# Kernel optimization log

Hardware: AMD Instinct MI355X
Metric: run time of the kernel (lower is better)

The kernel has to match this reference:

```python
import jax, jax.numpy as jnp
import numpy as np

CODEBOOK_DIM = 64
CODEBOOK_SLOTS = 512
TEMPERATURE = 0.5
BS, H, W = 16, 64, 64
EPS_G = 1e-10  # gumbel numerical floor
EPS_P = 1e-9   # matches probs.add(1e-09) in torch code


def setup_inputs() -> dict:
    key = jax.random.key(0)
    k1, k2, k3 = jax.random.split(key, 3)
    ze = jax.random.normal(k1, (BS, CODEBOOK_DIM, H, W), dtype=jnp.float32)
    codebook = jax.random.normal(k2, (CODEBOOK_SLOTS, CODEBOOK_DIM), dtype=jnp.float32)
    # uniform noise for Gumbel reparameterization of RelaxedOneHotCategorical.rsample
    u = jax.random.uniform(k3, (BS * H * W, CODEBOOK_SLOTS), dtype=jnp.float32)
    return {"ze": ze, "codebook": codebook, "u": u}


def reference(ze, codebook, u):
    bs, d, h, w = ze.shape
    K = codebook.shape[0]
    log_K = jnp.log(jnp.float32(K))
    # [bs, d, h, w] -> [N, d]
    ze_flat = jnp.transpose(ze, (0, 2, 3, 1)).reshape(-1, d)
    # squared euclidean distances via addmm: ||c||^2 + ||z||^2 - 2 z c^T  -> [N, K]
    distances = (
        jnp.sum(codebook * codebook, axis=1)[None, :]
        + jnp.sum(ze_flat * ze_flat, axis=1, keepdims=True)
        - 2.0 * (ze_flat @ codebook.T)
    )
    logits = -distances
    # Gumbel-softmax (relaxed one-hot categorical rsample)
    gumbel = -jnp.log(-jnp.log(u + EPS_G) + EPS_G)
    soft_onehot = jax.nn.softmax((logits + gumbel) / TEMPERATURE, axis=1)
    hard_indices = jnp.argmax(soft_onehot, axis=1).reshape(bs, h, w)
    # weighted codebook lookup: [N, K] @ [K, d] -> [bs, h, w, d] -> [bs, d, h, w]
    z_q = jnp.transpose((soft_onehot @ codebook).reshape(bs, h, w, d), (0, 3, 1, 2))
    probs = jax.nn.softmax(logits, axis=1)
    KL = jnp.mean(jnp.sum((probs * (jnp.log(probs + EPS_P) + log_K)).reshape(bs, -1), axis=1))
    commit_loss = jnp.mean(jnp.sum((probs * distances).reshape(bs, -1), axis=1))
    return (z_q, hard_indices, KL, commit_loss)
```

## Files before the change

### kernel.cpp

```cpp
#include <hip/hip_runtime.h>
#include <math.h>
#include <stdint.h>

#define IDX_OFF 4194304
#define KL_OFF  4259840
#define CM_OFF  4259841
#define LOG_K   6.238324625039508f
#define THR     2.0f

typedef _Float16 half8 __attribute__((ext_vector_type(8)));
typedef _Float16 half4 __attribute__((ext_vector_type(4)));
typedef float    f32x4 __attribute__((ext_vector_type(4)));

__global__ __launch_bounds__(64) void vq_pack(const float* __restrict__ cbk, void* __restrict__ ws){
  _Float16* LAh = (_Float16*)ws;
  _Float16* LAl = LAh + 32768;
  _Float16* QAh = LAl + 32768;
  float*    CCw = (float*)(QAh + 32768);
  const int slot = blockIdx.x, c = threadIdx.x;
  const float x = cbk[(slot << 6) + c];
  const _Float16 h = (_Float16)x;
  const _Float16 l = (_Float16)(x - (float)h);
  const int g = slot >> 4;
  {
    const int kc = c >> 5, quad = (c >> 3) & 3, j = c & 7;
    const int lane = (quad << 4) | (slot & 15);
    const int idx = ((((g << 1) | kc) << 6) | lane) * 8 + j;
    LAh[idx] = h; LAl[idx] = l;
  }
  {
    const int quad2 = (slot >> 2) & 3, j2 = slot & 3;
    const int cg = c >> 4;
    const int lane = (quad2 << 4) | (c & 15);
    QAh[(((g << 6) | lane) << 4) | (cg << 2) | j2] = h;
  }
  float s = x * x;
#pragma unroll
  for (int m = 1; m < 64; m <<= 1) s += __shfl_xor(s, m, 64);
  if (c == 0) CCw[slot] = s;
}

__global__ __launch_bounds__(512, 3) void vq_main(
    const float* __restrict__ ze, const float* __restrict__ uin,
    const void* __restrict__ ws, float* __restrict__ out)
{
  __shared__ float LX[4*22*64];
  __shared__ float RED[8];
  const _Float16* wsp = (const _Float16*)ws;
  const half8* LAh = (const half8*)wsp;
  const half8* LAl = (const half8*)(wsp + 32768);
  const half8* QA8 = (const half8*)(wsp + 65536);
  const float* CCw = (const float*)(wsp + 98304);

  const int tid  = threadIdx.x;
  const int lane = tid & 63, l15 = lane & 15, quad = lane >> 4;
  const int wv   = tid >> 6, pg = wv & 3, half = wv >> 2;
  const int n    = (blockIdx.x << 6) | (pg << 4) | l15;
  const int bb   = n >> 12, hh = (n >> 6) & 63, w = n & 63;

  const float* zp = ze + ((size_t)bb << 18) + (hh << 6) + w;
  half8 zh[2], zl[2];
  float zz = 0.f;
#pragma unroll
  for (int kc = 0; kc < 2; ++kc)
#pragma unroll
    for (int j = 0; j < 8; ++j){
      const float x = zp[(size_t)((kc << 5) + (quad << 3) + j) << 12];
      zz = fmaf(x, x, zz);
      const _Float16 h = (_Float16)x;
      zh[kc][j] = h;
      zl[kc][j] = (_Float16)(x - (float)h);
    }
  zz += __shfl_xor(zz, 16, 64);
  zz += __shfl_xor(zz, 32, 64);

  float m1 = -3.0e38f, s1 = 0.f, s2s = 0.f, t1s = 0.f, am = -3.0e38f;
  int   ki = 0;
  f32x4 zq0 = {0.f,0.f,0.f,0.f}, zq1 = {0.f,0.f,0.f,0.f};
  f32x4 zq2 = {0.f,0.f,0.f,0.f}, zq3 = {0.f,0.f,0.f,0.f};

  const float* uB = uin + ((size_t)n << 9) + (half << 8) + (quad << 2);
  const int gbase = half << 4;

#pragma unroll 2
  for (int g = 0; g < 16; ++g){
    const int gl = gbase + g;
    const float4 uf = *(const float4*)(uB + (g << 4));
    const float4 c4 = *(const float4*)(CCw + (gl << 4) + (quad << 2));
    const half8 ch0 = LAh[((gl << 1) | 0) * 64 + lane];
    const half8 ch1 = LAh[((gl << 1) | 1) * 64 + lane];
    const half8 cl0 = LAl[((gl << 1) | 0) * 64 + lane];
    const half8 cl1 = LAl[((gl << 1) | 1) * 64 + lane];
    const half8 qa01 = QA8[((gl << 6) | lane) * 2 + 0];
    const half8 qa23 = QA8[((gl << 6) | lane) * 2 + 1];

    f32x4 acc = {0.f,0.f,0.f,0.f};
    acc = __builtin_amdgcn_mfma_f32_16x16x32_f16(ch0, zh[0], acc, 0,0,0);
    acc = __builtin_amdgcn_mfma_f32_16x16x32_f16(cl0, zh[0], acc, 0,0,0);
    acc = __builtin_amdgcn_mfma_f32_16x16x32_f16(ch0, zl[0], acc, 0,0,0);
    acc = __builtin_amdgcn_mfma_f32_16x16x32_f16(ch1, zh[1], acc, 0,0,0);
    acc = __builtin_amdgcn_mfma_f32_16x16x32_f16(cl1, zh[1], acc, 0,0,0);
    acc = __builtin_amdgcn_mfma_f32_16x16x32_f16(ch1, zl[1], acc, 0,0,0);

    const float ua[4] = {uf.x, uf.y, uf.z, uf.w};
    const float ca[4] = {c4.x, c4.y, c4.z, c4.w};
    float lg[4], lu[4], av[4];
#pragma unroll
    for (int r = 0; r < 4; ++r){
      lg[r] = fmaf(2.f, acc[r], -ca[r] - zz);
      lu[r] = 1e-10f - __logf(ua[r] + 1e-10f);
      av[r] = lg[r] - __logf(lu[r]);
    }
    float pm = fmaxf(fmaxf(av[0], av[1]), fmaxf(av[2], av[3]));
    pm = fmaxf(pm, __shfl_xor(pm, 16, 64));
    pm = fmaxf(pm, __shfl_xor(pm, 32, 64));
    if (pm > m1 + THR){
      const float sc = __expf(m1 - pm), sc2 = sc * sc;
      s1 *= sc2; s2s *= sc; t1s *= sc;
      zq0 *= sc2; zq1 *= sc2; zq2 *= sc2; zq3 *= sc2;
      m1 = pm;
    }
    half4 ef;
    const int sb = (gl << 4) | (quad << 2);
#pragma unroll
    for (int r = 0; r < 4; ++r){
      const float t = __expf(av[r] - m1);
      const float e = t * t;
      s1 += e;
      ef[r] = (_Float16)e;
      const float p = t * lu[r];
      s2s += p;
      t1s = fmaf(p, lg[r], t1s);
      if (av[r] > am){ am = av[r]; ki = sb + r; }
    }
    const half4 qa0 = __builtin_shufflevector(qa01, qa01, 0,1,2,3);
    const half4 qa1 = __builtin_shufflevector(qa01, qa01, 4,5,6,7);
    const half4 qa2 = __builtin_shufflevector(qa23, qa23, 0,1,2,3);
    const half4 qa3 = __builtin_shufflevector(qa23, qa23, 4,5,6,7);
    zq0 = __builtin_amdgcn_mfma_f32_16x16x16f16(qa0, ef, zq0, 0,0,0);
    zq1 = __builtin_amdgcn_mfma_f32_16x16x16f16(qa1, ef, zq1, 0,0,0);
    zq2 = __builtin_amdgcn_mfma_f32_16x16x16f16(qa2, ef, zq2, 0,0,0);
    zq3 = __builtin_amdgcn_mfma_f32_16x16x16f16(qa3, ef, zq3, 0,0,0);
  }

#pragma unroll
  for (int m = 16; m < 64; m <<= 1){
    s1  += __shfl_xor(s1,  m, 64);
    s2s += __shfl_xor(s2s, m, 64);
    t1s += __shfl_xor(t1s, m, 64);
    const float vo = __shfl_xor(am, m, 64);
    const int   io = __shfl_xor(ki, m, 64);
    if (vo > am || (vo == am && io < ki)){ am = vo; ki = io; }
  }

  float* X = &LX[(pg * 22) * 64 + lane];
  if (half == 1){
#pragma unroll
    for (int r = 0; r < 4; ++r){
      X[(r     ) << 6] = zq0[r];
      X[(r +  4) << 6] = zq1[r];
      X[(r +  8) << 6] = zq2[r];
      X[(r + 12) << 6] = zq3[r];
    }
    X[16 << 6] = s1;  X[17 << 6] = s2s; X[18 << 6] = t1s;
    X[19 << 6] = m1;  X[20 << 6] = am;  X[21 << 6] = __int_as_float(ki);
  }
  __syncthreads();
  if (half == 0){
    const float m1B = X[19 << 6];
    const float M   = fmaxf(m1, m1B);
    const float sA  = __expf(m1 - M),  sB  = __expf(m1B - M);
    const float sA2 = sA * sA,         sB2 = sB * sB;
    s1  = s1  * sA2 + X[16 << 6] * sB2;
    s2s = s2s * sA  + X[17 << 6] * sB;
    t1s = t1s * sA  + X[18 << 6] * sB;
    const float amB = X[20 << 6];
    const int   kiB = __float_as_int(X[21 << 6]);
    if (amB > am || (amB == am && kiB < ki)){ am = amB; ki = kiB; }
    m1 = M;
#pragma unroll
    for (int r = 0; r < 4; ++r){
      zq0[r] = zq0[r] * sA2 + X[(r     ) << 6] * sB2;
      zq1[r] = zq1[r] * sA2 + X[(r +  4) << 6] * sB2;
      zq2[r] = zq2[r] * sA2 + X[(r +  8) << 6] * sB2;
      zq3[r] = zq3[r] * sA2 + X[(r + 12) << 6] * sB2;
    }

    const float inv = 1.0f / s1;
    const float pl  = t1s / s2s;
    float kl = pl + LOG_K - m1 - __logf(s2s);
    float cm = -pl;
    if (quad == 0) out[IDX_OFF + n] = (float)ki;

    float* ob = out + ((size_t)bb << 18) + (hh << 6) + w;
#pragma unroll
    for (int r = 0; r < 4; ++r){
      const int cb = (quad << 2) + r;
      ob[(size_t)(cb     ) << 12] = zq0[r] * inv;
      ob[(size_t)(cb + 16) << 12] = zq1[r] * inv;
      ob[(size_t)(cb + 32) << 12] = zq2[r] * inv;
      ob[(size_t)(cb + 48) << 12] = zq3[r] * inv;
    }

    if (quad != 0){ kl = 0.f; cm = 0.f; }
#pragma unroll
    for (int m = 1; m < 64; m <<= 1){ kl += __shfl_xor(kl, m, 64); cm += __shfl_xor(cm, m, 64); }
    if (lane == 0){ RED[pg] = kl; RED[pg + 4] = cm; }
  }
  __syncthreads();
  if (tid == 0){
    atomicAdd(out + KL_OFF, (RED[0]+RED[1]+RED[2]+RED[3]) * 0.0625f);
    atomicAdd(out + CM_OFF, (RED[4]+RED[5]+RED[6]+RED[7]) * 0.0625f);
  }
}

extern "C" void kernel_launch(void* const* d_in, const int* in_sizes, int n_in,
                              void* d_out, int out_size, void* d_ws, size_t ws_size,
                              hipStream_t stream){
  const float* ze  = (const float*)d_in[0];
  const float* cbk = (const float*)d_in[1];
  const float* uin = (const float*)d_in[2];
  float* out = (float*)d_out;
  hipMemsetAsync(out + KL_OFF, 0, 2 * sizeof(float), stream);
  vq_pack<<<dim3(512), dim3(64), 0, stream>>>(cbk, d_ws);
  vq_main<<<dim3(1024), dim3(512), 0, stream>>>(ze, uin, d_ws, out);
}
```

Before: 249.0 us.

## Software-pipeline codebook and noise loads and shrink blocks to 256 threads

Adds register double-buffering so each loop iteration already holds its codebook fragments and uniform noise, prefetching the next group's codebook data and the noise two groups ahead. Blocks now cover 32 points with 4 waves instead of 64 points with 8, and the grid doubles with adjusted launch bounds. The aim is to hide global/L2 load latency behind MFMA and transcendental work and to give the scheduler more, smaller blocks. In exchange it raises register pressure, which can cut occupancy, and the last iterations issue wrapped-around loads that are never used.

```diff
diff --git a/kernel.cpp b/kernel.cpp
--- a/kernel.cpp
+++ b/kernel.cpp
@@ -40,12 +40,12 @@
   if (c == 0) CCw[slot] = s;
 }
 
-__global__ __launch_bounds__(512, 3) void vq_main(
+__global__ __launch_bounds__(256, 4) void vq_main(
     const float* __restrict__ ze, const float* __restrict__ uin,
     const void* __restrict__ ws, float* __restrict__ out)
 {
-  __shared__ float LX[4*22*64];
-  __shared__ float RED[8];
+  __shared__ float LX[2*22*64];
+  __shared__ float RED[4];
   const _Float16* wsp = (const _Float16*)ws;
   const half8* LAh = (const half8*)wsp;
   const half8* LAl = (const half8*)(wsp + 32768);
@@ -54,8 +54,8 @@
 
   const int tid  = threadIdx.x;
   const int lane = tid & 63, l15 = lane & 15, quad = lane >> 4;
-  const int wv   = tid >> 6, pg = wv & 3, half = wv >> 2;
-  const int n    = (blockIdx.x << 6) | (pg << 4) | l15;
+  const int wv   = tid >> 6, pg = wv & 1, half = wv >> 1;
+  const int n    = (blockIdx.x << 5) | (pg << 4) | l15;
   const int bb   = n >> 12, hh = (n >> 6) & 63, w = n & 63;
 
   const float* zp = ze + ((size_t)bb << 18) + (hh << 6) + w;
@@ -82,28 +82,40 @@
   const float* uB = uin + ((size_t)n << 9) + (half << 8) + (quad << 2);
   const int gbase = half << 4;
 
-#pragma unroll 2
+  float4 ufc = *(const float4*)(uB);
+  float4 uf1 = *(const float4*)(uB + 16);
+  float4 c4c = *(const float4*)(CCw + (gbase << 4) + (quad << 2));
+  half8 ch0c = LAh[((gbase << 1) | 0) * 64 + lane];
+  half8 ch1c = LAh[((gbase << 1) | 1) * 64 + lane];
+  half8 cl0c = LAl[((gbase << 1) | 0) * 64 + lane];
+  half8 cl1c = LAl[((gbase << 1) | 1) * 64 + lane];
+  half8 qa01c = QA8[((gbase << 6) | lane) * 2 + 0];
+  half8 qa23c = QA8[((gbase << 6) | lane) * 2 + 1];
+
+#pragma unroll 4
   for (int g = 0; g < 16; ++g){
-    const int gl = gbase + g;
-    const float4 uf = *(const float4*)(uB + (g << 4));
-    const float4 c4 = *(const float4*)(CCw + (gl << 4) + (quad << 2));
-    const half8 ch0 = LAh[((gl << 1) | 0) * 64 + lane];
-    const half8 ch1 = LAh[((gl << 1) | 1) * 64 + lane];
-    const half8 cl0 = LAl[((gl << 1) | 0) * 64 + lane];
-    const half8 cl1 = LAl[((gl << 1) | 1) * 64 + lane];
-    const half8 qa01 = QA8[((gl << 6) | lane) * 2 + 0];
-    const half8 qa23 = QA8[((gl << 6) | lane) * 2 + 1];
+    const int g1 = (g + 1) & 15, g2 = (g + 2) & 15;
+    const int gl  = gbase + g;
+    const int gl1 = gbase + g1;
+    const float4 uf2 = *(const float4*)(uB + (g2 << 4));
+    const float4 c4n = *(const float4*)(CCw + (gl1 << 4) + (quad << 2));
+    const half8 ch0n = LAh[((gl1 << 1) | 0) * 64 + lane];
+    const half8 ch1n = LAh[((gl1 << 1) | 1) * 64 + lane];
+    const half8 cl0n = LAl[((gl1 << 1) | 0) * 64 + lane];
+    const half8 cl1n = LAl[((gl1 << 1) | 1) * 64 + lane];
+    const half8 qa01n = QA8[((gl1 << 6) | lane) * 2 + 0];
+    const half8 qa23n = QA8[((gl1 << 6) | lane) * 2 + 1];
 
     f32x4 acc = {0.f,0.f,0.f,0.f};
-    acc = __builtin_amdgcn_mfma_f32_16x16x32_f16(ch0, zh[0], acc, 0,0,0);
-    acc = __builtin_amdgcn_mfma_f32_16x16x32_f16(cl0, zh[0], acc, 0,0,0);
-    acc = __builtin_amdgcn_mfma_f32_16x16x32_f16(ch0, zl[0], acc, 0,0,0);
-    acc = __builtin_amdgcn_mfma_f32_16x16x32_f16(ch1, zh[1], acc, 0,0,0);
-    acc = __builtin_amdgcn_mfma_f32_16x16x32_f16(cl1, zh[1], acc, 0,0,0);
-    acc = __builtin_amdgcn_mfma_f32_16x16x32_f16(ch1, zl[1], acc, 0,0,0);
-
-    const float ua[4] = {uf.x, uf.y, uf.z, uf.w};
-    const float ca[4] = {c4.x, c4.y, c4.z, c4.w};
+    acc = __builtin_amdgcn_mfma_f32_16x16x32_f16(ch0c, zh[0], acc, 0,0,0);
+    acc = __builtin_amdgcn_mfma_f32_16x16x32_f16(cl0c, zh[0], acc, 0,0,0);
+    acc = __builtin_amdgcn_mfma_f32_16x16x32_f16(ch0c, zl[0], acc, 0,0,0);
+    acc = __builtin_amdgcn_mfma_f32_16x16x32_f16(ch1c, zh[1], acc, 0,0,0);
+    acc = __builtin_amdgcn_mfma_f32_16x16x32_f16(cl1c, zh[1], acc, 0,0,0);
+    acc = __builtin_amdgcn_mfma_f32_16x16x32_f16(ch1c, zl[1], acc, 0,0,0);
+
+    const float ua[4] = {ufc.x, ufc.y, ufc.z, ufc.w};
+    const float ca[4] = {c4c.x, c4c.y, c4c.z, c4c.w};
     float lg[4], lu[4], av[4];
 #pragma unroll
     for (int r = 0; r < 4; ++r){
@@ -133,14 +145,18 @@
       t1s = fmaf(p, lg[r], t1s);
       if (av[r] > am){ am = av[r]; ki = sb + r; }
     }
-    const half4 qa0 = __builtin_shufflevector(qa01, qa01, 0,1,2,3);
-    const half4 qa1 = __builtin_shufflevector(qa01, qa01, 4,5,6,7);
-    const half4 qa2 = __builtin_shufflevector(qa23, qa23, 0,1,2,3);
-    const half4 qa3 = __builtin_shufflevector(qa23, qa23, 4,5,6,7);
+    const half4 qa0 = __builtin_shufflevector(qa01c, qa01c, 0,1,2,3);
+    const half4 qa1 = __builtin_shufflevector(qa01c, qa01c, 4,5,6,7);
+    const half4 qa2 = __builtin_shufflevector(qa23c, qa23c, 0,1,2,3);
+    const half4 qa3 = __builtin_shufflevector(qa23c, qa23c, 4,5,6,7);
     zq0 = __builtin_amdgcn_mfma_f32_16x16x16f16(qa0, ef, zq0, 0,0,0);
     zq1 = __builtin_amdgcn_mfma_f32_16x16x16f16(qa1, ef, zq1, 0,0,0);
     zq2 = __builtin_amdgcn_mfma_f32_16x16x16f16(qa2, ef, zq2, 0,0,0);
     zq3 = __builtin_amdgcn_mfma_f32_16x16x16f16(qa3, ef, zq3, 0,0,0);
+
+    ufc = uf1; uf1 = uf2; c4c = c4n;
+    ch0c = ch0n; ch1c = ch1n; cl0c = cl0n; cl1c = cl1n;
+    qa01c = qa01n; qa23c = qa23n;
   }
 
 #pragma unroll
@@ -205,12 +221,12 @@
     if (quad != 0){ kl = 0.f; cm = 0.f; }
 #pragma unroll
     for (int m = 1; m < 64; m <<= 1){ kl += __shfl_xor(kl, m, 64); cm += __shfl_xor(cm, m, 64); }
-    if (lane == 0){ RED[pg] = kl; RED[pg + 4] = cm; }
+    if (lane == 0){ RED[pg] = kl; RED[pg + 2] = cm; }
   }
   __syncthreads();
   if (tid == 0){
-    atomicAdd(out + KL_OFF, (RED[0]+RED[1]+RED[2]+RED[3]) * 0.0625f);
-    atomicAdd(out + CM_OFF, (RED[4]+RED[5]+RED[6]+RED[7]) * 0.0625f);
+    atomicAdd(out + KL_OFF, (RED[0] + RED[1]) * 0.0625f);
+    atomicAdd(out + CM_OFF, (RED[2] + RED[3]) * 0.0625f);
   }
 }
 
@@ -223,5 +239,5 @@
   float* out = (float*)d_out;
   hipMemsetAsync(out + KL_OFF, 0, 2 * sizeof(float), stream);
   vq_pack<<<dim3(512), dim3(64), 0, stream>>>(cbk, d_ws);
-  vq_main<<<dim3(1024), dim3(512), 0, stream>>>(ze, uin, d_ws, out);
+  vq_main<<<dim3(2048), dim3(256), 0, stream>>>(ze, uin, d_ws, out);
 }
```

Result: slower. 370.9 us (+49.0%).
